# Kernel tuning notes

Hardware: AMD Instinct MI355X
Metric: run time of the kernel (lower is better)

Reference implementation:

```python
import jax, jax.numpy as jnp
import numpy as np

NUM_LAYERS = 4
NUM_BINS = 16
TAIL_BOUND = 3.0
MIN_BIN_WIDTH = 1e-3
MIN_BIN_HEIGHT = 1e-3
MIN_DERIVATIVE = 1e-3
PARAMS_PER_LAYER = 3 * NUM_BINS - 1  # 47


def setup_inputs() -> dict:
    key = jax.random.key(0)
    k1, k2 = jax.random.split(key)
    B, T, D = 32, 512, 32
    params = jax.random.normal(k1, (B, T, D, NUM_LAYERS * PARAMS_PER_LAYER), dtype=jnp.float32)
    x = jax.random.normal(k2, (B, T, D), dtype=jnp.float32)
    return {"params": params, "x": x}


def _gather(t, idx):
    # t: [..., K], idx: [...] -> [...]
    return jnp.take_along_axis(t, idx[..., None], axis=-1)[..., 0]


def _rqs_forward(x, uw, uh, ud):
    """Unconstrained rational-quadratic spline, forward (inverse=False), linear tails.
    x: [...], uw/uh: [..., K], ud: [..., K-1]. Returns (y, log|dy/dx|) elementwise."""
    K = NUM_BINS
    TB = TAIL_BOUND
    inside = (x >= -TB) & (x <= TB)
    # pad derivatives so boundary slope = min_derivative + softplus(const) = 1
    const = float(np.log(np.expm1(1.0 - MIN_DERIVATIVE)))
    ud = jnp.pad(ud, [(0, 0)] * (ud.ndim - 1) + [(1, 1)], constant_values=const)

    widths = MIN_BIN_WIDTH + (1.0 - MIN_BIN_WIDTH * K) * jax.nn.softmax(uw, axis=-1)
    cw = jnp.cumsum(widths, axis=-1)
    cw = jnp.pad(cw, [(0, 0)] * (cw.ndim - 1) + [(1, 0)])
    cw = 2.0 * TB * cw - TB
    cw = cw.at[..., 0].set(-TB).at[..., -1].set(TB)  # exact endpoints
    widths = cw[..., 1:] - cw[..., :-1]

    derivs = MIN_DERIVATIVE + jax.nn.softplus(ud)  # [..., K+1]

    heights = MIN_BIN_HEIGHT + (1.0 - MIN_BIN_HEIGHT * K) * jax.nn.softmax(uh, axis=-1)
    ch = jnp.cumsum(heights, axis=-1)
    ch = jnp.pad(ch, [(0, 0)] * (ch.ndim - 1) + [(1, 0)])
    ch = 2.0 * TB * ch - TB
    ch = ch.at[..., 0].set(-TB).at[..., -1].set(TB)
    heights = ch[..., 1:] - ch[..., :-1]

    xc = jnp.clip(x, -TB, TB)
    # searchsorted: index of bin containing xc
    idx = jnp.clip(jnp.sum((xc[..., None] >= cw).astype(jnp.int32), axis=-1) - 1, 0, K - 1)

    xk = _gather(cw[..., :-1], idx)
    wk = _gather(widths, idx)
    yk = _gather(ch[..., :-1], idx)
    hk = _gather(heights, idx)
    dk = _gather(derivs[..., :-1], idx)
    dk1 = _gather(derivs[..., 1:], idx)

    delta = hk / wk
    theta = (xc - xk) / wk
    t1m = theta * (1.0 - theta)
    denom = delta + (dk + dk1 - 2.0 * delta) * t1m
    y = yk + hk * (delta * theta * theta + dk * t1m) / denom
    dnum = delta * delta * (dk1 * theta * theta + 2.0 * delta * t1m + dk * (1.0 - theta) ** 2)
    ld = jnp.log(dnum) - 2.0 * jnp.log(denom)

    return jnp.where(inside, y, x), jnp.where(inside, ld, jnp.zeros_like(ld))


def reference(params, x):
    logdet = jnp.zeros(x.shape[0], dtype=x.dtype)
    for li in range(NUM_LAYERS):
        o = li * PARAMS_PER_LAYER
        uw = params[..., o:o + NUM_BINS]
        uh = params[..., o + NUM_BINS:o + 2 * NUM_BINS]
        ud = params[..., o + 2 * NUM_BINS:o + 3 * NUM_BINS - 1]
        x, ld = _rqs_forward(x, uw, uh, ud)
        logdet = logdet + ld.sum(axis=tuple(range(1, ld.ndim)))
    return x, logdet
```

## Files before the change

kernel.cpp:

```cpp
#include <hip/hip_runtime.h>

static constexpr int   KBINS = 16;
static constexpr float TB    = 3.0f;
static constexpr float MIN_W = 0.001f;
static constexpr float MIN_H = 0.001f;
static constexpr float MIN_D = 0.001f;
static constexpr int   PPL   = 47;
static constexpr int   REC_F4 = 47;

__device__ __forceinline__ float softplusf(float v) {
  return fmaxf(v, 0.0f) + __logf(1.0f + __expf(-fabsf(v)));
}

template<int F0, int N>
__device__ __forceinline__ void extractAbs(const float4* ch, float* a) {
#pragma unroll
  for (int k = 0; k < N; ++k) {
    const int f = F0 + k;
    const float4 q = ch[f >> 2];
    const int c = f & 3;
    a[k] = (c == 0) ? q.x : (c == 1) ? q.y : (c == 2) ? q.z : q.w;
  }
}

template<int LI>
__device__ __forceinline__ void computeLayer(const float4* ch, float& x, float& ldsum) {
  const float xc = fminf(fmaxf(x, -TB), TB);

  float uw[KBINS];
  extractAbs<LI * PPL, KBINS>(ch, uw);
  float s = 0.0f;
#pragma unroll
  for (int k = 0; k < KBINS; ++k) { uw[k] = __expf(uw[k]); s += uw[k]; }
  const float csw = (1.0f - KBINS * MIN_W) / s;

  float cum = 0.0f, ek = -TB;
  float xk = -TB, xk1 = TB;
  int idx = 0;
#pragma unroll
  for (int k = 0; k < KBINS; ++k) {
    cum += fmaf(uw[k], csw, MIN_W);
    const float ek1 = (k == KBINS - 1) ? TB : fmaf(2.0f * TB, cum, -TB);
    if (xc >= ek) { idx = k; xk = ek; xk1 = ek1; }
    ek = ek1;
  }
  const float wk = xk1 - xk;

  float uh[KBINS];
  extractAbs<LI * PPL + KBINS, KBINS>(ch, uh);
  s = 0.0f;
#pragma unroll
  for (int k = 0; k < KBINS; ++k) { uh[k] = __expf(uh[k]); s += uh[k]; }
  const float csh = (1.0f - KBINS * MIN_H) / s;

  cum = 0.0f; ek = -TB;
  float yk = -TB, yk1 = TB;
#pragma unroll
  for (int k = 0; k < KBINS; ++k) {
    cum += fmaf(uh[k], csh, MIN_H);
    const float ek1 = (k == KBINS - 1) ? TB : fmaf(2.0f * TB, cum, -TB);
    if (k == idx) { yk = ek; yk1 = ek1; }
    ek = ek1;
  }
  const float hk = yk1 - yk;

  float ud[KBINS - 1];
  extractAbs<LI * PPL + 2 * KBINS, KBINS - 1>(ch, ud);
  float udk = 0.0f, udk1 = 0.0f;
#pragma unroll
  for (int j = 0; j < KBINS - 1; ++j) {
    if (j == idx - 1) udk  = ud[j];
    if (j == idx)     udk1 = ud[j];
  }
  const float dk  = (idx == 0)         ? 1.0f : MIN_D + softplusf(udk);
  const float dk1 = (idx == KBINS - 1) ? 1.0f : MIN_D + softplusf(udk1);

  const float rw    = 1.0f / wk;
  const float delta = hk * rw;
  const float theta = (xc - xk) * rw;
  const float omt   = 1.0f - theta;
  const float t1m   = theta * omt;
  const float denom = delta + (dk + dk1 - 2.0f * delta) * t1m;
  const float y     = yk + hk * (delta * theta * theta + dk * t1m) / denom;
  const float dnum  = (delta * delta) *
                      (dk1 * theta * theta + 2.0f * delta * t1m + dk * omt * omt);
  const float ld    = __logf(dnum) - 2.0f * __logf(denom);

  const bool inside = (x >= -TB) && (x <= TB);
  x      = inside ? y : x;
  ldsum += inside ? ld : 0.0f;
}

__global__ __launch_bounds__(256, 2) void nsf_flow_burst(
    const float* __restrict__ params, const float* __restrict__ xin,
    float* __restrict__ yout, float* __restrict__ logdet, int epb) {
  const int e = blockIdx.x * 256 + threadIdx.x;
  const float4* p4 = reinterpret_cast<const float4*>(params) + (size_t)e * REC_F4;

  float4 ch[REC_F4];
#pragma unroll
  for (int j = 0; j < REC_F4; ++j) ch[j] = p4[j];
  float x = xin[e];

  float ldsum = 0.0f;
  computeLayer<0>(ch, x, ldsum);
  computeLayer<1>(ch, x, ldsum);
  computeLayer<2>(ch, x, ldsum);
  computeLayer<3>(ch, x, ldsum);

  yout[e] = x;

  float v = ldsum;
#pragma unroll
  for (int o = 32; o > 0; o >>= 1) v += __shfl_xor(v, o, 64);
  __shared__ float red[4];
  const int wid = threadIdx.x >> 6;
  if ((threadIdx.x & 63) == 0) red[wid] = v;
  __syncthreads();
  if (threadIdx.x == 0) {
    const int b = e / epb;
    atomicAdd(&logdet[b], red[0] + red[1] + red[2] + red[3]);
  }
}

extern "C" void kernel_launch(void* const* d_in, const int* in_sizes, int n_in,
                              void* d_out, int out_size, void* d_ws, size_t ws_size,
                              hipStream_t stream) {
  const float* params = (const float*)d_in[0];
  const float* x      = (const float*)d_in[1];
  const int n   = in_sizes[1];
  const int nb  = out_size - n;
  const int epb = n / nb;
  float* y      = (float*)d_out;
  float* logdet = y + n;

  hipMemsetAsync(logdet, 0, nb * sizeof(float), stream);
  nsf_flow_burst<<<dim3(n / 256), dim3(256), 0, stream>>>(params, x, y, logdet, epb);
}
```

Measured before the change: 85.19 us.

## Split each element across a quad of lanes with shuffle-based scans

Each spline element is now handled by four cooperating lanes instead of one thread. Each lane loads interleaved float4 chunks of the 47-float4 record, which makes the loads coalesced and cuts per-thread registers from 47 float4 to 12. Softmax sums, cumulative sums, the bin search and the gathers are combined across the quad with shuffles. Occupancy is raised through launch bounds 3. The cost is four times as many threads, duplicated per-element arithmetic, and extra shuffle latency.

Result: slower. 123.0 us (+44.3%).

```diff
diff --git a/kernel.cpp b/kernel.cpp
--- a/kernel.cpp
+++ b/kernel.cpp
@@ -6,74 +6,198 @@
 static constexpr float MIN_H = 0.001f;
 static constexpr float MIN_D = 0.001f;
 static constexpr int   PPL   = 47;
-static constexpr int   REC_F4 = 47;
 
 __device__ __forceinline__ float softplusf(float v) {
   return fmaxf(v, 0.0f) + __logf(1.0f + __expf(-fabsf(v)));
 }
 
-template<int F0, int N>
-__device__ __forceinline__ void extractAbs(const float4* ch, float* a) {
-#pragma unroll
-  for (int k = 0; k < N; ++k) {
-    const int f = F0 + k;
-    const float4 q = ch[f >> 2];
-    const int c = f & 3;
-    a[k] = (c == 0) ? q.x : (c == 1) ? q.y : (c == 2) ? q.z : q.w;
-  }
+__device__ __forceinline__ float comp(const float4& q, int t) {
+  return (t == 0) ? q.x : (t == 1) ? q.y : (t == 2) ? q.z : q.w;
+}
+
+__device__ __forceinline__ void quadScan(float v, int cq, float& excl, float& tot) {
+  float inc = v;
+  float u1 = __shfl_up(inc, 1, 4); inc += (cq >= 1) ? u1 : 0.0f;
+  float u2 = __shfl_up(inc, 2, 4); inc += (cq >= 2) ? u2 : 0.0f;
+  excl = inc - v;
+  tot  = __shfl(inc, 3, 4);
+}
+
+template<int GW0, int S0, int S1>
+__device__ __forceinline__ void widthSearch(const float4* ch, int cq, float xc,
+                                            int& idx, float& xk, float& wk) {
+  constexpr bool TWO = (S1 != S0);
+  const int c4 = cq * 4;
+  float eA[4], eB[4];
+  float sA = 0.0f, sB = 0.0f;
+#pragma unroll
+  for (int t = 0; t < 4; ++t) {
+    const int rel = c4 + (16 * S0 + t - GW0);
+    const bool in = (rel >= 0) && (rel < 16);
+    const float e = in ? __expf(comp(ch[S0], t)) : 0.0f;
+    eA[t] = e; sA += e;
+  }
+  if constexpr (TWO) {
+#pragma unroll
+    for (int t = 0; t < 4; ++t) {
+      const int rel = c4 + (16 * S1 + t - GW0);
+      const bool in = (rel >= 0) && (rel < 16);
+      const float e = in ? __expf(comp(ch[S1], t)) : 0.0f;
+      eB[t] = e; sB += e;
+    }
+  }
+  float bA, tA, bB = 0.0f, tBt = 0.0f;
+  quadScan(sA, cq, bA, tA);
+  if constexpr (TWO) quadScan(sB, cq, bB, tBt);
+  const float csw = (1.0f - KBINS * MIN_W) / (tA + tBt);
+
+  int   brel = -1;
+  float bxk = 0.0f, bwk = 1.0f;
+  float cum = bA;
+#pragma unroll
+  for (int t = 0; t < 4; ++t) {
+    const int rel = c4 + (16 * S0 + t - GW0);
+    const bool in = (rel >= 0) && (rel < 16);
+    const float cumL = cum; cum += eA[t];
+    const float eL = (rel == 0)  ? -TB : fmaf(6.0f, fmaf(csw, cumL, MIN_W * rel), -TB);
+    const float eR = (rel == 15) ?  TB : fmaf(6.0f, fmaf(csw, cum, MIN_W * (rel + 1)), -TB);
+    const bool val = in && (xc >= eL);
+    brel = val ? rel : brel;
+    bxk  = val ? eL  : bxk;
+    bwk  = val ? (eR - eL) : bwk;
+  }
+  if constexpr (TWO) {
+    cum = tA + bB;
+#pragma unroll
+    for (int t = 0; t < 4; ++t) {
+      const int rel = c4 + (16 * S1 + t - GW0);
+      const bool in = (rel >= 0) && (rel < 16);
+      const float cumL = cum; cum += eB[t];
+      const float eL = (rel == 0)  ? -TB : fmaf(6.0f, fmaf(csw, cumL, MIN_W * rel), -TB);
+      const float eR = (rel == 15) ?  TB : fmaf(6.0f, fmaf(csw, cum, MIN_W * (rel + 1)), -TB);
+      const bool val = in && (xc >= eL);
+      brel = val ? rel : brel;
+      bxk  = val ? eL  : bxk;
+      bwk  = val ? (eR - eL) : bwk;
+    }
+  }
+#pragma unroll
+  for (int d = 1; d <= 2; d <<= 1) {
+    const int   orel = __shfl_xor(brel, d);
+    const float oxk  = __shfl_xor(bxk, d);
+    const float owk  = __shfl_xor(bwk, d);
+    const bool take = orel > brel;
+    brel = take ? orel : brel;
+    bxk  = take ? oxk  : bxk;
+    bwk  = take ? owk  : bwk;
+  }
+  idx = brel; xk = bxk; wk = bwk;
+}
+
+template<int GW0, int S0, int S1>
+__device__ __forceinline__ void heightGather(const float4* ch, int cq, int idx,
+                                             float& yk, float& hk) {
+  constexpr bool TWO = (S1 != S0);
+  const int c4 = cq * 4;
+  float eA[4], eB[4];
+  float sA = 0.0f, sB = 0.0f;
+#pragma unroll
+  for (int t = 0; t < 4; ++t) {
+    const int rel = c4 + (16 * S0 + t - GW0);
+    const bool in = (rel >= 0) && (rel < 16);
+    const float e = in ? __expf(comp(ch[S0], t)) : 0.0f;
+    eA[t] = e; sA += e;
+  }
+  if constexpr (TWO) {
+#pragma unroll
+    for (int t = 0; t < 4; ++t) {
+      const int rel = c4 + (16 * S1 + t - GW0);
+      const bool in = (rel >= 0) && (rel < 16);
+      const float e = in ? __expf(comp(ch[S1], t)) : 0.0f;
+      eB[t] = e; sB += e;
+    }
+  }
+  float bA, tA, bB = 0.0f, tBt = 0.0f;
+  quadScan(sA, cq, bA, tA);
+  if constexpr (TWO) quadScan(sB, cq, bB, tBt);
+  const float csh = (1.0f - KBINS * MIN_H) / (tA + tBt);
+
+  float ykc = 0.0f, yk1c = 0.0f;
+  float cum = bA;
+#pragma unroll
+  for (int t = 0; t < 4; ++t) {
+    const int rel = c4 + (16 * S0 + t - GW0);
+    const bool in = (rel >= 0) && (rel < 16);
+    const float cumL = cum; cum += eA[t];
+    const float eL = (rel == 0)  ? -TB : fmaf(6.0f, fmaf(csh, cumL, MIN_H * rel), -TB);
+    const float eR = (rel == 15) ?  TB : fmaf(6.0f, fmaf(csh, cum, MIN_H * (rel + 1)), -TB);
+    const bool match = in && (rel == idx);
+    ykc  += match ? eL : 0.0f;
+    yk1c += match ? eR : 0.0f;
+  }
+  if constexpr (TWO) {
+    cum = tA + bB;
+#pragma unroll
+    for (int t = 0; t < 4; ++t) {
+      const int rel = c4 + (16 * S1 + t - GW0);
+      const bool in = (rel >= 0) && (rel < 16);
+      const float cumL = cum; cum += eB[t];
+      const float eL = (rel == 0)  ? -TB : fmaf(6.0f, fmaf(csh, cumL, MIN_H * rel), -TB);
+      const float eR = (rel == 15) ?  TB : fmaf(6.0f, fmaf(csh, cum, MIN_H * (rel + 1)), -TB);
+      const bool match = in && (rel == idx);
+      ykc  += match ? eL : 0.0f;
+      yk1c += match ? eR : 0.0f;
+    }
+  }
+  ykc  += __shfl_xor(ykc, 1);  ykc  += __shfl_xor(ykc, 2);
+  yk1c += __shfl_xor(yk1c, 1); yk1c += __shfl_xor(yk1c, 2);
+  yk = ykc; hk = yk1c - ykc;
+}
+
+template<int GW0, int S0, int S1>
+__device__ __forceinline__ void derivGather(const float4* ch, int cq, int idx,
+                                            float& dk, float& dk1) {
+  const int c4 = cq * 4;
+  float a0 = 0.0f, a1 = 0.0f;
+#pragma unroll
+  for (int t = 0; t < 4; ++t) {
+    const int rel = c4 + (16 * S0 + t - GW0);
+    const bool in = (rel >= 0) && (rel < 15);
+    const float v = comp(ch[S0], t);
+    a0 += (in && (rel == idx - 1)) ? v : 0.0f;
+    a1 += (in && (rel == idx))     ? v : 0.0f;
+  }
+  if constexpr (S1 != S0) {
+#pragma unroll
+    for (int t = 0; t < 4; ++t) {
+      const int rel = c4 + (16 * S1 + t - GW0);
+      const bool in = (rel >= 0) && (rel < 15);
+      const float v = comp(ch[S1], t);
+      a0 += (in && (rel == idx - 1)) ? v : 0.0f;
+      a1 += (in && (rel == idx))     ? v : 0.0f;
+    }
+  }
+  a0 += __shfl_xor(a0, 1); a0 += __shfl_xor(a0, 2);
+  a1 += __shfl_xor(a1, 1); a1 += __shfl_xor(a1, 2);
+  dk  = (idx == 0)         ? 1.0f : MIN_D + softplusf(a0);
+  dk1 = (idx == KBINS - 1) ? 1.0f : MIN_D + softplusf(a1);
 }
 
 template<int LI>
-__device__ __forceinline__ void computeLayer(const float4* ch, float& x, float& ldsum) {
+__device__ __forceinline__ void layer(const float4* ch, int cq, float& x, float& ldsum) {
+  constexpr int F0  = LI * PPL;
+  constexpr int SW0 = F0 >> 4,        SW1 = (F0 + 15) >> 4;
+  constexpr int SH0 = (F0 + 16) >> 4, SH1 = (F0 + 31) >> 4;
+  constexpr int SD0 = (F0 + 32) >> 4, SD1 = (F0 + 46) >> 4;
+
   const float xc = fminf(fmaxf(x, -TB), TB);
 
-  float uw[KBINS];
-  extractAbs<LI * PPL, KBINS>(ch, uw);
-  float s = 0.0f;
-#pragma unroll
-  for (int k = 0; k < KBINS; ++k) { uw[k] = __expf(uw[k]); s += uw[k]; }
-  const float csw = (1.0f - KBINS * MIN_W) / s;
-
-  float cum = 0.0f, ek = -TB;
-  float xk = -TB, xk1 = TB;
-  int idx = 0;
-#pragma unroll
-  for (int k = 0; k < KBINS; ++k) {
-    cum += fmaf(uw[k], csw, MIN_W);
-    const float ek1 = (k == KBINS - 1) ? TB : fmaf(2.0f * TB, cum, -TB);
-    if (xc >= ek) { idx = k; xk = ek; xk1 = ek1; }
-    ek = ek1;
-  }
-  const float wk = xk1 - xk;
-
-  float uh[KBINS];
-  extractAbs<LI * PPL + KBINS, KBINS>(ch, uh);
-  s = 0.0f;
-#pragma unroll
-  for (int k = 0; k < KBINS; ++k) { uh[k] = __expf(uh[k]); s += uh[k]; }
-  const float csh = (1.0f - KBINS * MIN_H) / s;
-
-  cum = 0.0f; ek = -TB;
-  float yk = -TB, yk1 = TB;
-#pragma unroll
-  for (int k = 0; k < KBINS; ++k) {
-    cum += fmaf(uh[k], csh, MIN_H);
-    const float ek1 = (k == KBINS - 1) ? TB : fmaf(2.0f * TB, cum, -TB);
-    if (k == idx) { yk = ek; yk1 = ek1; }
-    ek = ek1;
-  }
-  const float hk = yk1 - yk;
-
-  float ud[KBINS - 1];
-  extractAbs<LI * PPL + 2 * KBINS, KBINS - 1>(ch, ud);
-  float udk = 0.0f, udk1 = 0.0f;
-#pragma unroll
-  for (int j = 0; j < KBINS - 1; ++j) {
-    if (j == idx - 1) udk  = ud[j];
-    if (j == idx)     udk1 = ud[j];
-  }
-  const float dk  = (idx == 0)         ? 1.0f : MIN_D + softplusf(udk);
-  const float dk1 = (idx == KBINS - 1) ? 1.0f : MIN_D + softplusf(udk1);
+  int idx; float xk, wk;
+  widthSearch<F0, SW0, SW1>(ch, cq, xc, idx, xk, wk);
+  float yk, hk;
+  heightGather<F0 + 16, SH0, SH1>(ch, cq, idx, yk, hk);
+  float dk, dk1;
+  derivGather<F0 + 32, SD0, SD1>(ch, cq, idx, dk, dk1);
 
   const float rw    = 1.0f / wk;
   const float delta = hk * rw;
@@ -91,36 +215,39 @@
   ldsum += inside ? ld : 0.0f;
 }
 
-__global__ __launch_bounds__(256, 2) void nsf_flow_burst(
+__global__ __launch_bounds__(256, 3) void nsf_quad(
     const float* __restrict__ params, const float* __restrict__ xin,
-    float* __restrict__ yout, float* __restrict__ logdet, int epb) {
-  const int e = blockIdx.x * 256 + threadIdx.x;
-  const float4* p4 = reinterpret_cast<const float4*>(params) + (size_t)e * REC_F4;
-
-  float4 ch[REC_F4];
-#pragma unroll
-  for (int j = 0; j < REC_F4; ++j) ch[j] = p4[j];
-  float x = xin[e];
+    float* __restrict__ yout, float* __restrict__ logdet, int bpb) {
+  const int l  = threadIdx.x;
+  const int cq = l & 3;
+  const int r  = blockIdx.x * 64 + (l >> 2);
+  const float4* p4 = reinterpret_cast<const float4*>(params) + (size_t)r * PPL;
+
+  float x = xin[r];
+  float4 ch[12];
+#pragma unroll
+  for (int i = 0; i < 11; ++i) ch[i] = p4[cq + 4 * i];
+  {
+    int cc = cq + 44; cc = (cc > 46) ? 46 : cc;
+    ch[11] = p4[cc];
+  }
 
   float ldsum = 0.0f;
-  computeLayer<0>(ch, x, ldsum);
-  computeLayer<1>(ch, x, ldsum);
-  computeLayer<2>(ch, x, ldsum);
-  computeLayer<3>(ch, x, ldsum);
-
-  yout[e] = x;
-
-  float v = ldsum;
+  layer<0>(ch, cq, x, ldsum);
+  layer<1>(ch, cq, x, ldsum);
+  layer<2>(ch, cq, x, ldsum);
+  layer<3>(ch, cq, x, ldsum);
+
+  if (cq == 0) yout[r] = x;
+
+  float v = (cq == 0) ? ldsum : 0.0f;
 #pragma unroll
   for (int o = 32; o > 0; o >>= 1) v += __shfl_xor(v, o, 64);
   __shared__ float red[4];
-  const int wid = threadIdx.x >> 6;
-  if ((threadIdx.x & 63) == 0) red[wid] = v;
+  const int wid = l >> 6;
+  if ((l & 63) == 0) red[wid] = v;
   __syncthreads();
-  if (threadIdx.x == 0) {
-    const int b = e / epb;
-    atomicAdd(&logdet[b], red[0] + red[1] + red[2] + red[3]);
-  }
+  if (l == 0) atomicAdd(&logdet[blockIdx.x / bpb], red[0] + red[1] + red[2] + red[3]);
 }
 
 extern "C" void kernel_launch(void* const* d_in, const int* in_sizes, int n_in,
@@ -131,9 +258,11 @@
   const int n   = in_sizes[1];
   const int nb  = out_size - n;
   const int epb = n / nb;
+  const int blocks = n / 64;
+  const int bpb    = epb / 64;
   float* y      = (float*)d_out;
   float* logdet = y + n;
 
   hipMemsetAsync(logdet, 0, nb * sizeof(float), stream);
-  nsf_flow_burst<<<dim3(n / 256), dim3(256), 0, stream>>>(params, x, y, logdet, epb);
-}
+  nsf_quad<<<dim3(blocks), dim3(256), 0, stream>>>(params, x, y, logdet, bpb);
+}
```
